# Kernel optimization log

Measured on AMD Instinct MI355X. Metric: run time of the kernel, lower is better.

The kernel has to match this reference:

```python
import jax, jax.numpy as jnp
import numpy as np

NHEAD = 12
EPS_Z = 1e-5
EPS_LN = 1e-5


def _zscore_last(t, n):
    # torch .std is unbiased (ddof=1)
    m = t.mean(axis=-1, keepdims=True)
    var = ((t - m) ** 2).sum(axis=-1, keepdims=True) / (n - 1)
    return (t - m) / (jnp.sqrt(var) + EPS_Z)


def _layernorm(x, g, b):
    m = x.mean(axis=-1, keepdims=True)
    v = ((x - m) ** 2).mean(axis=-1, keepdims=True)
    return (x - m) * jax.lax.rsqrt(v + EPS_LN) * g + b


def setup_inputs() -> dict:
    key = jax.random.key(0)
    ks = jax.random.split(key, 20)
    B, T, D, FF, E = 2, 1024, 768, 3072, 4
    p = lambda k, shape: (jax.random.normal(k, shape, jnp.float32) * 0.02)
    return {
        "src": jax.random.normal(ks[0], (B, T, D), jnp.float32),
        "frac": jax.random.uniform(ks[1], (B, T), jnp.float32),
        "Wq": p(ks[2], (D, D)), "bq": jnp.zeros((D,), jnp.float32),
        "Wk": p(ks[3], (D, D)), "bk": jnp.zeros((D,), jnp.float32),
        "Wv": p(ks[4], (D, D)), "bv": jnp.zeros((D,), jnp.float32),
        "Wo": p(ks[5], (D, D)), "bo": jnp.zeros((D,), jnp.float32),
        "gamma": jnp.float32(1.0),
        "ln1_g": jnp.ones((D,), jnp.float32), "ln1_b": jnp.zeros((D,), jnp.float32),
        "ln2_g": jnp.ones((D,), jnp.float32), "ln2_b": jnp.zeros((D,), jnp.float32),
        "Wg": p(ks[6], (E, D)), "bg": jnp.zeros((E,), jnp.float32),
        "W1": p(ks[7], (E, D, FF)), "b1": jnp.zeros((E, FF), jnp.float32),
        "W2": p(ks[8], (E, FF, D)), "b2": jnp.zeros((E, D), jnp.float32),
    }


def reference(src, frac, Wq, bq, Wk, bk, Wv, bv, Wo, bo, gamma,
              ln1_g, ln1_b, ln2_g, ln2_b, Wg, bg, W1, b1, W2, b2):
    B, T, D = src.shape
    H = NHEAD
    hd = D // H
    scale = hd ** -0.5

    # ---- attention (add_frac_bias=False path) ----
    Q = (src @ Wq.T + bq).reshape(B, T, H, hd)
    K = (src @ Wk.T + bk).reshape(B, T, H, hd)
    V = (src @ Wv.T + bv).reshape(B, T, H, hd)
    logits = jnp.einsum('bqhd,bkhd->bhqk', Q, K) * scale
    logits = gamma * _zscore_last(logits, T)
    probs = jax.nn.softmax(logits, axis=-1)
    attn = jnp.einsum('bhqk,bkhd->bqhd', probs, V).reshape(B, T, D)
    attn = attn @ Wo.T + bo

    # ---- residual + norm1 ----
    x = _layernorm(src + attn, ln1_g, ln1_b)

    # ---- MoE top-2 feed-forward ----
    E = Wg.shape[0]
    gate_scores = jax.nn.softmax(x @ Wg.T + bg, axis=-1)          # [B,T,E]
    top2_val, top2_idx = jax.lax.top_k(gate_scores, 2)            # [B,T,2]
    combine = (jax.nn.one_hot(top2_idx, E, dtype=x.dtype)
               * top2_val[..., None]).sum(axis=-2)                # [B,T,E]
    h = jax.nn.relu(jnp.einsum('btd,edf->ebtf', x, W1) + b1[:, None, None, :])
    y = jnp.einsum('ebtf,efd->ebtd', h, W2) + b2[:, None, None, :]
    ff = jnp.einsum('ebtd,bte->btd', y, combine)

    # ---- residual + norm2 ----
    return _layernorm(x + ff, ln2_g, ln2_b)
```

## Files before the change

kernel.cpp:

```cpp
#include <hip/hip_runtime.h>

typedef unsigned short u16;
typedef short bf16x8 __attribute__((ext_vector_type(8)));
typedef float f32x4 __attribute__((ext_vector_type(4)));

#define BB 2
#define TT 1024
#define DD 768
#define HH 12
#define HD 64
#define FFD 3072
#define NE 4
#define NTOK (BB*TT)
#define CROWS 4608
#define SLABZ 3538944L

#define MFMA16(a, b, c) __builtin_amdgcn_mfma_f32_16x16x32_bf16((a), (b), (c), 0, 0, 0)

#define ASYNC16(gsrc, ldst)                                                    \
    __builtin_amdgcn_global_load_lds(                                          \
        (const __attribute__((address_space(1))) void*)(gsrc),                 \
        (__attribute__((address_space(3))) void*)(ldst), 16, 0, 0)

__device__ __forceinline__ float us2f(u16 u) {
    return __uint_as_float(((unsigned int)u) << 16);
}
__device__ __forceinline__ u16 f2us(float f) {
    unsigned int x = __float_as_uint(f);
    x += 0x7fffu + ((x >> 16) & 1u);
    return (u16)(x >> 16);
}

__global__ __launch_bounds__(256) void convert5_kernel(
    const float* __restrict__ src, const float* __restrict__ wq,
    const float* __restrict__ wk, const float* __restrict__ wv,
    const float* __restrict__ wo,
    const float* __restrict__ bq, const float* __restrict__ bk,
    const float* __restrict__ bv,
    u16* __restrict__ src_h, u16* __restrict__ wqkv_h, u16* __restrict__ wo_h,
    float* __restrict__ bqkv)
{
    const int bid = blockIdx.x, tid = threadIdx.x;
    if (bid == 1920) {
        for (int i = tid; i < 3 * DD; i += 256) {
            float v = (i < DD) ? bq[i] : (i < 2 * DD) ? bk[i - DD] : bv[i - 2 * DD];
            bqkv[i] = v;
        }
        return;
    }
    int i = bid * 256 + tid;
    const float* in; u16* out; int off;
    if (i < 196608) { in = src; out = src_h; off = i; }
    else {
        int j = i - 196608; int w = j / 73728; off = j - w * 73728;
        in = (w == 0) ? wq : (w == 1) ? wk : (w == 2) ? wv : wo;
        out = (w < 3) ? wqkv_h + (size_t)w * (DD * DD) : wo_h;
    }
    const float4* p = reinterpret_cast<const float4*>(in) + (size_t)off * 2;
    float4 a = p[0], b = p[1];
    u16 o[8] = {f2us(a.x), f2us(a.y), f2us(a.z), f2us(a.w),
                f2us(b.x), f2us(b.y), f2us(b.z), f2us(b.w)};
    *reinterpret_cast<uint4*>(out + (size_t)off * 8) = *reinterpret_cast<uint4*>(o);
}

__global__ __launch_bounds__(256) void transpose_convert_kernel(
    const float* __restrict__ src, u16* __restrict__ dst,
    int C, int dstStride, long srcZ, long dstZ)
{
    __shared__ float tile[32][33];
    const float* s = src + (size_t)blockIdx.z * srcZ;
    u16* d = dst + (size_t)blockIdx.z * dstZ;
    const int c0 = blockIdx.x * 32, r0 = blockIdx.y * 32;
    const int tid = threadIdx.x;
    {
        const int r = tid >> 3, cs = (tid & 7) * 4;
        float4 v = *reinterpret_cast<const float4*>(&s[(size_t)(r0 + r) * C + c0 + cs]);
        tile[r][cs] = v.x; tile[r][cs + 1] = v.y;
        tile[r][cs + 2] = v.z; tile[r][cs + 3] = v.w;
    }
    __syncthreads();
    {
        const int c = tid >> 3, rs = (tid & 7) * 4;
        u16 o[4] = {f2us(tile[rs][c]), f2us(tile[rs + 1][c]),
                    f2us(tile[rs + 2][c]), f2us(tile[rs + 3][c])};
        *reinterpret_cast<uint2*>(&d[(size_t)(c0 + c) * dstStride + r0 + rs]) =
            *reinterpret_cast<uint2*>(o);
    }
}

__global__ __launch_bounds__(256) void scan_build_kernel(
    const int* __restrict__ epack, int* __restrict__ cnt,
    int* __restrict__ rowtok, int* __restrict__ tok2row)
{
    __shared__ int sc[256][4];
    const int tid = threadIdx.x;
    for (int i = tid; i < CROWS; i += 256) rowtok[i] = 0;
    int ep[8];
    int l0 = 0, l1 = 0, l2 = 0, l3 = 0;
    #pragma unroll
    for (int i = 0; i < 8; i++) {
        const int v = epack[tid * 8 + i];
        ep[i] = v;
        const int a = v & 15, b = (v >> 4) & 15;
        l0 += (a == 0) + (b == 0);
        l1 += (a == 1) + (b == 1);
        l2 += (a == 2) + (b == 2);
        l3 += (a == 3) + (b == 3);
    }
    sc[tid][0] = l0; sc[tid][1] = l1; sc[tid][2] = l2; sc[tid][3] = l3;
    __syncthreads();
    for (int off = 1; off < 256; off <<= 1) {
        int v0 = 0, v1 = 0, v2 = 0, v3 = 0;
        if (tid >= off) {
            v0 = sc[tid - off][0]; v1 = sc[tid - off][1];
            v2 = sc[tid - off][2]; v3 = sc[tid - off][3];
        }
        __syncthreads();
        if (tid >= off) {
            sc[tid][0] += v0; sc[tid][1] += v1;
            sc[tid][2] += v2; sc[tid][3] += v3;
        }
        __syncthreads();
    }
    const int t0 = sc[255][0], t1 = sc[255][1], t2 = sc[255][2], t3 = sc[255][3];
    if (tid == 0) { cnt[0] = t0; cnt[1] = t1; cnt[2] = t2; cnt[3] = t3; }
    const int b1 = (t0 + 127) & ~127;
    const int b2 = b1 + ((t1 + 127) & ~127);
    const int b3 = b2 + ((t2 + 127) & ~127);
    int r0 = sc[tid][0] - l0;
    int r1 = b1 + sc[tid][1] - l1;
    int r2 = b2 + sc[tid][2] - l2;
    int r3 = b3 + sc[tid][3] - l3;
    #pragma unroll
    for (int i = 0; i < 8; i++) {
        const int t = tid * 8 + i;
        const int a = ep[i] & 15, b = (ep[i] >> 4) & 15;
        const int ra = (a == 0) ? r0++ : (a == 1) ? r1++ : (a == 2) ? r2++ : r3++;
        rowtok[ra] = t; tok2row[t * 2] = ra;
        const int rb = (b == 0) ? r0++ : (b == 1) ? r1++ : (b == 2) ? r2++ : r3++;
        rowtok[rb] = t; tok2row[t * 2 + 1] = rb;
    }
}

__global__ __launch_bounds__(256) void gemm_bt_kernel(
    const u16* __restrict__ A, int lda, long aZ,
    const u16* __restrict__ Bt, int ldb, long bZ,
    int K, int mode, int swz,
    float* __restrict__ outF, u16* __restrict__ outH,
    u16* __restrict__ outH2, u16* __restrict__ outH3,
    int ldc, long cZ,
    const float* __restrict__ biasF, int biasZ,
    const int* __restrict__ rowtok, const int* __restrict__ cntp,
    const float* __restrict__ comb)
{
    __shared__ __align__(16) u16 As[128 * 64];
    __shared__ __align__(16) u16 Bs[128 * 64];
    const int tid = threadIdx.x;
    int bx, by, z, e = 0, baseE = 0;
    if (swz == 3) {
        const int fid = blockIdx.x;
        const int xcd = fid & 7; int r = fid >> 3;
        const int half = (r >= 96) ? 1 : 0; r -= half * 96;
        bx = r % 6; by = r / 6;
        const int ez = xcd * 2 + half; e = ez >> 2; z = ez & 3;
    } else if (swz == 1) {
        const int fid = blockIdx.x;
        const int xcd = fid & 7; const int r = fid >> 3;
        const int ne = xcd * 12 + (r % 12);
        by = r / 12; bx = ne % 24; e = ne / 24; z = e;
    } else {
        bx = blockIdx.x; by = blockIdx.y; z = blockIdx.z;
    }
    if (mode == 2 || mode == 4) {
        const int q0 = (cntp[0] + 127) & ~127;
        const int q1 = (cntp[1] + 127) & ~127;
        const int q2 = (cntp[2] + 127) & ~127;
        baseE = (e > 0 ? q0 : 0) + (e > 1 ? q1 : 0) + (e > 2 ? q2 : 0);
        if (by * 128 >= cntp[e]) return;
    }
    const int m0 = by * 128, n0 = bx * 128;
    const u16* Ab = A + (size_t)z * aZ;
    const u16* Bb = Bt + (size_t)z * bZ;
    if (mode == 4) {
        Ab += (size_t)baseE * lda;
        Bb += (size_t)e * ((size_t)DD * FFD);
    }

    const int wave = tid >> 6, lane = tid & 63;
    const int wm = (wave & 1) * 64, wn = (wave >> 1) * 64;
    const int fm = lane & 15;
    const int g  = lane >> 4;

    const int lr8 = lane >> 3;
    const int cg  = ((lane & 7) ^ lr8) * 8;
    const u16 *aG[4], *bG[4];
    u16 *aL[4], *bL[4];
    #pragma unroll
    for (int i = 0; i < 4; i++) {
        const int rr = wave * 32 + i * 8 + lr8;
        int arow;
        if (mode == 2) arow = rowtok[baseE + m0 + rr];
        else           arow = m0 + rr;
        aG[i] = Ab + (size_t)arow * lda + cg;
        bG[i] = Bb + (size_t)(n0 + rr) * ldb + cg;
        aL[i] = &As[(wave * 32 + i * 8) * 64];
        bL[i] = &Bs[(wave * 32 + i * 8) * 64];
    }

    const int c0 = ((g    ) ^ (fm & 7)) * 8;
    const int c1 = ((g + 4) ^ (fm & 7)) * 8;
    const u16* pa[4]; const u16* pb[4];
    #pragma unroll
    for (int i = 0; i < 4; i++) {
        pa[i] = &As[(wm + i * 16 + fm) * 64];
        pb[i] = &Bs[(wn + i * 16 + fm) * 64];
    }

    f32x4 acc[4][4] = {};

    for (int k0 = 0; k0 < K; k0 += 64) {
        #pragma unroll
        for (int i = 0; i < 4; i++) ASYNC16(aG[i] + k0, aL[i]);
        #pragma unroll
        for (int i = 0; i < 4; i++) ASYNC16(bG[i] + k0, bL[i]);
        __syncthreads();
        #pragma unroll
        for (int ks = 0; ks < 2; ks++) {
            const int cc = ks ? c1 : c0;
            bf16x8 af[4], bf[4];
            #pragma unroll
            for (int i = 0; i < 4; i++)
                af[i] = *reinterpret_cast<const bf16x8*>(pa[i] + cc);
            #pragma unroll
            for (int j = 0; j < 4; j++)
                bf[j] = *reinterpret_cast<const bf16x8*>(pb[j] + cc);
            #pragma unroll
            for (int i = 0; i < 4; i++)
                #pragma unroll
                for (int j = 0; j < 4; j++)
                    acc[i][j] = MFMA16(af[i], bf[j], acc[i][j]);
        }
        __syncthreads();
    }

    const int cn = lane & 15, cr = (lane >> 4) * 4;

    if (mode == 2) {
        u16* Cs = As;
        #pragma unroll
        for (int i = 0; i < 4; i++) {
            if (i) __syncthreads();
            int tokr[4]; float combr[4];
            #pragma unroll
            for (int r = 0; r < 4; r++)
                tokr[r] = rowtok[baseE + m0 + wm + i * 16 + cr + r];
            #pragma unroll
            for (int r = 0; r < 4; r++)
                combr[r] = comb[(size_t)tokr[r] * NE + z];
            #pragma unroll
            for (int j = 0; j < 4; j++) {
                const int n = n0 + wn + j * 16 + cn;
                const float bias = biasF[(size_t)z * biasZ + n];
                #pragma unroll
                for (int r = 0; r < 4; r++) {
                    float y = fmaxf(acc[i][j][r] + bias, 0.f) * combr[r];
                    Cs[((wave & 1) * 16 + cr + r) * 128 + wn + j * 16 + cn] = f2us(y);
                }
            }
            __syncthreads();
            const int lr2 = tid >> 3, c2 = (tid & 7) * 16;
            const int m2 = m0 + (lr2 >> 4) * 64 + i * 16 + (lr2 & 15);
            u16* dst = outH + (size_t)(baseE + m2) * ldc + n0 + c2;
            *reinterpret_cast<uint4*>(dst) =
                *reinterpret_cast<const uint4*>(&Cs[lr2 * 128 + c2]);
            *reinterpret_cast<uint4*>(dst + 8) =
                *reinterpret_cast<const uint4*>(&Cs[lr2 * 128 + c2 + 8]);
        }
        return;
    }

    #pragma unroll
    for (int i = 0; i < 4; i++) {
        #pragma unroll
        for (int j = 0; j < 4; j++) {
            const int n = n0 + wn + j * 16 + cn;
            #pragma unroll
            for (int r = 0; r < 4; r++) {
                const int m = m0 + wm + i * 16 + cr + r;
                float y = acc[i][j][r];
                if (mode == 0) {
                    y += biasF[n];
                    int which = (n >= 1536) ? 2 : (n >= 768 ? 1 : 0);
                    int nn = n - which * 768;
                    int bb = m >> 10, t = m & 1023;
                    int hh = nn >> 6, d = nn & 63;
                    if (which == 0)
                        outH[(((size_t)(bb * HH + hh) * TT + t) << 6) + d] = f2us(y);
                    else if (which == 1)
                        outH2[(((size_t)(bb * HH + hh) * TT + t) << 6) + d] = f2us(y);
                    else
                        outH3[(((size_t)(bb * HH + hh) * HD + d) << 10) + t] = f2us(y);
                } else {
                    float* basep = outF + (size_t)z * cZ;
                    basep[(size_t)(baseE + m) * ldc + n] = y;
                }
            }
        }
    }
}

#define PSTR 1032
__global__ __launch_bounds__(256, 2) void attn_mfma_kernel(
    const u16* __restrict__ Qh, const u16* __restrict__ Kh,
    const u16* __restrict__ VT, const float* __restrict__ gamma_p,
    u16* __restrict__ attn_out)
{
    __shared__ __align__(16) u16 P[32 * PSTR];
    __shared__ float wred[4][32][4];
    __shared__ float dred[4][32];
    __shared__ float aArr[32], cmArr[32], dinvArr[32];

    const int qt = blockIdx.x, bh = blockIdx.y;
    const int b = bh / HH, h = bh - b * HH;
    const int tid = threadIdx.x, wave = tid >> 6, lane = tid & 63;
    const int g = lane >> 4, fm = lane & 15;
    const float gamma = gamma_p[0];
    const int m0 = qt * 32;
    const u16* Qp = Qh + (size_t)bh * TT * HD;
    const u16* Kp = Kh + (size_t)bh * TT * HD;
    const u16* Vp = VT + (size_t)bh * HD * TT;

    bf16x8 af[2][2];
    #pragma unroll
    for (int mi = 0; mi < 2; mi++)
        #pragma unroll
        for (int ks = 0; ks < 2; ks++)
            af[mi][ks] = *reinterpret_cast<const bf16x8*>(
                Qp + (size_t)(m0 + mi * 16 + fm) * HD + ks * 32 + g * 8);

    const int n0w = wave * 256;
    f32x4 acc[16][2] = {};
    #pragma unroll
    for (int nj = 0; nj < 16; nj++) {
        const u16* kp = Kp + (size_t)(n0w + nj * 16 + fm) * HD + g * 8;
        bf16x8 b0 = *reinterpret_cast<const bf16x8*>(kp);
        bf16x8 b1 = *reinterpret_cast<const bf16x8*>(kp + 32);
        acc[nj][0] = MFMA16(af[0][0], b0, acc[nj][0]);
        acc[nj][0] = MFMA16(af[0][1], b1, acc[nj][0]);
        acc[nj][1] = MFMA16(af[1][0], b0, acc[nj][1]);
        acc[nj][1] = MFMA16(af[1][1], b1, acc[nj][1]);
    }

    #pragma unroll
    for (int mi = 0; mi < 2; mi++) {
        #pragma unroll
        for (int r = 0; r < 4; r++) {
            float s1 = 0.f, s2 = 0.f, mx = -3.4e38f, mn = 3.4e38f;
            #pragma unroll
            for (int nj = 0; nj < 16; nj++) {
                float v = acc[nj][mi][r];
                s1 += v; s2 = fmaf(v, v, s2);
                mx = fmaxf(mx, v); mn = fminf(mn, v);
            }
            #pragma unroll
            for (int msk = 1; msk < 16; msk <<= 1) {
                s1 += __shfl_xor(s1, msk);
                s2 += __shfl_xor(s2, msk);
                mx = fmaxf(mx, __shfl_xor(mx, msk));
                mn = fminf(mn, __shfl_xor(mn, msk));
            }
            if (fm == 0) {
                int row = mi * 16 + g * 4 + r;
                wred[wave][row][0] = s1; wred[wave][row][1] = s2;
                wred[wave][row][2] = mx; wred[wave][row][3] = mn;
            }
        }
    }
    __syncthreads();
    if (tid < 32) {
        float s1 = 0.f, s2 = 0.f, mx = -3.4e38f, mn = 3.4e38f;
        #pragma unroll
        for (int w = 0; w < 4; w++) {
            s1 += wred[w][tid][0]; s2 += wred[w][tid][1];
            mx = fmaxf(mx, wred[w][tid][2]); mn = fminf(mn, wred[w][tid][3]);
        }
        float var = (s2 - s1 * s1 * (1.f / TT)) * (1.f / (TT - 1));
        var = fmaxf(var, 0.f);
        float a = gamma / (sqrtf(var) + 8e-5f);
        aArr[tid] = a;
        cmArr[tid] = (a >= 0.f) ? a * mx : a * mn;
    }
    __syncthreads();

    #pragma unroll
    for (int mi = 0; mi < 2; mi++) {
        #pragma unroll
        for (int r = 0; r < 4; r++) {
            const int row = mi * 16 + g * 4 + r;
            const float a = aArr[row], cm = cmArr[row];
            float dp = 0.f;
            #pragma unroll
            for (int nj = 0; nj < 16; nj++) {
                float p = __expf(fmaf(a, acc[nj][mi][r], -cm));
                u16 pb = f2us(p);
                dp += us2f(pb);
                P[row * PSTR + n0w + nj * 16 + fm] = pb;
            }
            #pragma unroll
            for (int msk = 1; msk < 16; msk <<= 1) dp += __shfl_xor(dp, msk);
            if (fm == 0) dred[wave][row] = dp;
        }
    }
    __syncthreads();
    if (tid < 32)
        dinvArr[tid] = 1.f / (dred[0][tid] + dred[1][tid] + dred[2][tid] + dred[3][tid]);
    __syncthreads();

    f32x4 oacc[2] = {};
    #pragma unroll 4
    for (int ks = 0; ks < 32; ks++) {
        bf16x8 bv = *reinterpret_cast<const bf16x8*>(
            Vp + (size_t)(wave * 16 + fm) * TT + ks * 32 + g * 8);
        bf16x8 a0 = *reinterpret_cast<const bf16x8*>(&P[(size_t)fm * PSTR + ks * 32 + g * 8]);
        bf16x8 a1 = *reinterpret_cast<const bf16x8*>(&P[(size_t)(16 + fm) * PSTR + ks * 32 + g * 8]);
        oacc[0] = MFMA16(a0, bv, oacc[0]);
        oacc[1] = MFMA16(a1, bv, oacc[1]);
    }
    #pragma unroll
    for (int mi = 0; mi < 2; mi++) {
        #pragma unroll
        for (int r = 0; r < 4; r++) {
            int row = mi * 16 + g * 4 + r;
            int t = m0 + row;
            attn_out[((size_t)(b * TT + t)) * DD + h * HD + wave * 16 + fm] =
                f2us(oacc[mi][r] * dinvArr[row]);
        }
    }
}

__global__ __launch_bounds__(256) void ln1_kernel(
    const float* __restrict__ p0, const float* __restrict__ p1,
    const float* __restrict__ p2, const float* __restrict__ p3,
    const float* __restrict__ src, const float* __restrict__ bo,
    const float* __restrict__ g, const float* __restrict__ bta,
    const float* __restrict__ Wg, const float* __restrict__ bg,
    float* __restrict__ outF, u16* __restrict__ outH,
    float* __restrict__ comb, int* __restrict__ epack)
{
    const int row = blockIdx.x, tid = threadIdx.x;
    __shared__ float red[256];
    __shared__ float gred[4][4];
    const size_t base = (size_t)row * DD;
    float v[3];
    #pragma unroll
    for (int i = 0; i < 3; i++) {
        int c = tid + i * 256;
        v[i] = p0[base + c] + p1[base + c] + p2[base + c] + p3[base + c]
             + src[base + c] + bo[c];
    }
    float s = v[0] + v[1] + v[2];
    red[tid] = s; __syncthreads();
    #pragma unroll
    for (int o = 128; o > 0; o >>= 1) { if (tid < o) red[tid] += red[tid + o]; __syncthreads(); }
    const float mean = red[0] * (1.f / 768.f);
    __syncthreads();
    float qv = 0.f;
    #pragma unroll
    for (int i = 0; i < 3; i++) { float d = v[i] - mean; qv += d * d; }
    red[tid] = qv; __syncthreads();
    #pragma unroll
    for (int o = 128; o > 0; o >>= 1) { if (tid < o) red[tid] += red[tid + o]; __syncthreads(); }
    const float var = red[0] * (1.f / 768.f);
    const float rs = rsqrtf(var + 1e-5f);
    float ga0 = 0.f, ga1 = 0.f, ga2 = 0.f, ga3 = 0.f;
    #pragma unroll
    for (int i = 0; i < 3; i++) {
        int c = tid + i * 256;
        float o = (v[i] - mean) * rs * g[c] + bta[c];
        outF[base + c] = o;
        outH[base + c] = f2us(o);
        ga0 = fmaf(o, Wg[c], ga0);
        ga1 = fmaf(o, Wg[DD + c], ga1);
        ga2 = fmaf(o, Wg[2 * DD + c], ga2);
        ga3 = fmaf(o, Wg[3 * DD + c], ga3);
    }
    #pragma unroll
    for (int off = 32; off > 0; off >>= 1) {
        ga0 += __shfl_down(ga0, off, 64);
        ga1 += __shfl_down(ga1, off, 64);
        ga2 += __shfl_down(ga2, off, 64);
        ga3 += __shfl_down(ga3, off, 64);
    }
    const int wave = tid >> 6, lane = tid & 63;
    if (lane == 0) {
        gred[wave][0] = ga0; gred[wave][1] = ga1;
        gred[wave][2] = ga2; gred[wave][3] = ga3;
    }
    __syncthreads();
    if (tid == 0) {
        float gg[NE];
        #pragma unroll
        for (int e = 0; e < NE; e++)
            gg[e] = gred[0][e] + gred[1][e] + gred[2][e] + gred[3][e] + bg[e];
        float m = -1e30f;
        #pragma unroll
        for (int e = 0; e < NE; e++) m = fmaxf(m, gg[e]);
        float ex[NE], ssum = 0.f;
        #pragma unroll
        for (int e = 0; e < NE; e++) { ex[e] = __expf(gg[e] - m); ssum += ex[e]; }
        #pragma unroll
        for (int e = 0; e < NE; e++) ex[e] /= ssum;
        int e1 = 0;
        #pragma unroll
        for (int e = 1; e < NE; e++) if (ex[e] > ex[e1]) e1 = e;
        int e2 = -1;
        #pragma unroll
        for (int e = 0; e < NE; e++) if (e != e1 && (e2 < 0 || ex[e] > ex[e2])) e2 = e;
        float c[NE] = {0.f, 0.f, 0.f, 0.f};
        c[e1] = ex[e1]; c[e2] = ex[e2];
        #pragma unroll
        for (int e = 0; e < NE; e++) comb[(size_t)row * NE + e] = c[e];
        epack[row] = e1 | (e2 << 4);
    }
}

__global__ __launch_bounds__(256) void ln2_kernel(
    const float* __restrict__ x, const float* __restrict__ pslab,
    const int* __restrict__ tok2row,
    const float* __restrict__ comb, const float* __restrict__ b2,
    const float* __restrict__ g, const float* __restrict__ bta,
    float* __restrict__ outF)
{
    const int row = blockIdx.x, tid = threadIdx.x;
    __shared__ float red[256];
    const size_t base = (size_t)row * DD;
    const int r0 = tok2row[row * 2], r1 = tok2row[row * 2 + 1];
    const float* q0 = pslab + (size_t)r0 * DD;
    const float* q1 = pslab + (size_t)r1 * DD;
    const float c0 = comb[row * NE + 0], c1 = comb[row * NE + 1];
    const float c2 = comb[row * NE + 2], c3 = comb[row * NE + 3];
    float v[3];
    #pragma unroll
    for (int i = 0; i < 3; i++) {
        int c = tid + i * 256;
        float t = x[base + c];
        t += q0[c] + q0[SLABZ + c] + q0[2 * SLABZ + c] + q0[3 * SLABZ + c];
        t += q1[c] + q1[SLABZ + c] + q1[2 * SLABZ + c] + q1[3 * SLABZ + c];
        t = fmaf(c0, b2[c], t);
        t = fmaf(c1, b2[DD + c], t);
        t = fmaf(c2, b2[2 * DD + c], t);
        t = fmaf(c3, b2[3 * DD + c], t);
        v[i] = t;
    }
    float s = v[0] + v[1] + v[2];
    red[tid] = s; __syncthreads();
    #pragma unroll
    for (int o = 128; o > 0; o >>= 1) { if (tid < o) red[tid] += red[tid + o]; __syncthreads(); }
    const float mean = red[0] * (1.f / 768.f);
    __syncthreads();
    float qv = 0.f;
    #pragma unroll
    for (int i = 0; i < 3; i++) { float d = v[i] - mean; qv += d * d; }
    red[tid] = qv; __syncthreads();
    #pragma unroll
    for (int o = 128; o > 0; o >>= 1) { if (tid < o) red[tid] += red[tid + o]; __syncthreads(); }
    const float var = red[0] * (1.f / 768.f);
    const float rs = rsqrtf(var + 1e-5f);
    #pragma unroll
    for (int i = 0; i < 3; i++) {
        int c = tid + i * 256;
        outF[base + c] = (v[i] - mean) * rs * g[c] + bta[c];
    }
}

extern "C" void kernel_launch(void* const* d_in, const int* in_sizes, int n_in,
                              void* d_out, int out_size, void* d_ws, size_t ws_size,
                              hipStream_t stream)
{
    const float* src  = (const float*)d_in[0];
    const float* Wq   = (const float*)d_in[2];  const float* bq = (const float*)d_in[3];
    const float* Wk   = (const float*)d_in[4];  const float* bk = (const float*)d_in[5];
    const float* Wv   = (const float*)d_in[6];  const float* bv = (const float*)d_in[7];
    const float* Wo   = (const float*)d_in[8];  const float* bo = (const float*)d_in[9];
    const float* gam  = (const float*)d_in[10];
    const float* ln1g = (const float*)d_in[11]; const float* ln1b = (const float*)d_in[12];
    const float* ln2g = (const float*)d_in[13]; const float* ln2b = (const float*)d_in[14];
    const float* Wg   = (const float*)d_in[15]; const float* bg = (const float*)d_in[16];
    const float* W1   = (const float*)d_in[17]; const float* b1 = (const float*)d_in[18];
    const float* W2   = (const float*)d_in[19]; const float* b2 = (const float*)d_in[20];
    (void)ws_size; (void)in_sizes; (void)n_in; (void)out_size;

    char* ws = (char*)d_ws;
    u16*   W1T  = (u16*)(ws);
    float* wop  = (float*)(ws + 18874368);
    float* pslab= (float*)(ws);
    u16*   W2T  = (u16*)(ws + 56623104);
    u16*   hb   = (u16*)(ws + 75497472);
    float* x    = (float*)(ws + 103809024);
    u16*   xh   = (u16*)(ws + 110100480);
    float* comb = (float*)(ws + 113246208);
    float* bqkv = (float*)(ws + 113278976);
    int*   cnt    = (int*)(ws + 113288192);
    int*   rowtok = (int*)(ws + 113288256);
    int*   epack  = (int*)(ws + 113306688);
    int*   tok2row= (int*)(ws + 113323072);
    char* H = ws + 75497472;
    u16*   Qh     = (u16*)(H);
    u16*   Kh     = (u16*)(H + 3145728);
    u16*   VTh    = (u16*)(H + 6291456);
    u16*   src_h  = (u16*)(H + 9437184);
    u16*   attn_h = (u16*)(H + 12582912);
    u16*   WqkvH  = (u16*)(H + 15728640);
    u16*   WoH    = (u16*)(H + 19267584);
    const long PZ = (long)NTOK * DD;

    convert5_kernel<<<1921, 256, 0, stream>>>(
        src, Wq, Wk, Wv, Wo, bq, bk, bv, src_h, WqkvH, WoH, bqkv);
    transpose_convert_kernel<<<dim3(FFD / 32, DD / 32, NE), 256, 0, stream>>>(
        W1, W1T, FFD, DD, (long)DD * FFD, (long)FFD * DD);
    transpose_convert_kernel<<<dim3(DD / 32, FFD / 32, NE), 256, 0, stream>>>(
        W2, W2T, DD, FFD, (long)FFD * DD, (long)FFD * DD);

    gemm_bt_kernel<<<dim3(2304 / 128, NTOK / 128, 1), 256, 0, stream>>>(
        src_h, DD, 0, WqkvH, DD, 0, DD, 0, 0,
        nullptr, Qh, Kh, VTh, 0, 0, bqkv, 0, nullptr, nullptr, nullptr);

    attn_mfma_kernel<<<dim3(TT / 32, BB * HH), 256, 0, stream>>>(
        Qh, Kh, VTh, gam, attn_h);

    gemm_bt_kernel<<<dim3(DD / 128, NTOK / 128, 4), 256, 0, stream>>>(
        attn_h, DD, 192L, WoH, DD, 192L, 192, 3, 0,
        wop, nullptr, nullptr, nullptr, DD, PZ, nullptr, 0, nullptr, nullptr, nullptr);

    ln1_kernel<<<NTOK, 256, 0, stream>>>(
        wop, wop + PZ, wop + 2 * PZ, wop + 3 * PZ, src, bo,
        ln1g, ln1b, Wg, bg, x, xh, comb, epack);

    scan_build_kernel<<<1, 256, 0, stream>>>(epack, cnt, rowtok, tok2row);

    gemm_bt_kernel<<<dim3(1536, 1, 1), 256, 0, stream>>>(
        xh, DD, 0, W1T, DD, (long)FFD * DD, DD, 2, 1,
        nullptr, hb, nullptr, nullptr, FFD, 0, b1, FFD, rowtok, cnt, comb);

    gemm_bt_kernel<<<dim3(1536, 1, 1), 256, 0, stream>>>(
        hb, FFD, 768L, W2T, FFD, 768L, 768, 4, 3,
        pslab, nullptr, nullptr, nullptr, DD, SLABZ, nullptr, 0, rowtok, cnt, nullptr);

    ln2_kernel<<<NTOK, 256, 0, stream>>>(
        x, pslab, tok2row, comb, b2, ln2g, ln2b, (float*)d_out);
}
```

Before: 369.5 us.

## Double-buffer LDS in QKV/out-proj GEMMs, coalesce QKV epilogue, XCD-aware tile mapping

Result: faster. 343.6 us (-7.0%).

```diff
diff --git a/kernel.cpp b/kernel.cpp
--- a/kernel.cpp
+++ b/kernel.cpp
@@ -142,6 +142,7 @@
     }
 }
 
+template<int DB>
 __global__ __launch_bounds__(256) void gemm_bt_kernel(
     const u16* __restrict__ A, int lda, long aZ,
     const u16* __restrict__ Bt, int ldb, long bZ,
@@ -153,8 +154,8 @@
     const int* __restrict__ rowtok, const int* __restrict__ cntp,
     const float* __restrict__ comb)
 {
-    __shared__ __align__(16) u16 As[128 * 64];
-    __shared__ __align__(16) u16 Bs[128 * 64];
+    __shared__ __align__(16) u16 As[(DB ? 2 : 1) * 128 * 64];
+    __shared__ __align__(16) u16 Bs[(DB ? 2 : 1) * 128 * 64];
     const int tid = threadIdx.x;
     int bx, by, z, e = 0, baseE = 0;
     if (swz == 3) {
@@ -168,6 +169,10 @@
         const int xcd = fid & 7; const int r = fid >> 3;
         const int ne = xcd * 12 + (r % 12);
         by = r / 12; bx = ne % 24; e = ne / 24; z = e;
+    } else if (swz == 2) {
+        const int fid = blockIdx.x;
+        const int g = (fid & 7) * 36 + (fid >> 3);
+        by = g & 15; bx = g >> 4; z = 0;
     } else {
         bx = blockIdx.x; by = blockIdx.y; z = blockIdx.z;
     }
@@ -207,6 +212,14 @@
         bL[i] = &Bs[(wave * 32 + i * 8) * 64];
     }
 
+#define STAGE(B, KO) do {                                                      \
+        const int _o = (B) * (128 * 64);                                       \
+        _Pragma("unroll")                                                      \
+        for (int _i = 0; _i < 4; _i++) ASYNC16(aG[_i] + (KO), aL[_i] + _o);    \
+        _Pragma("unroll")                                                      \
+        for (int _i = 0; _i < 4; _i++) ASYNC16(bG[_i] + (KO), bL[_i] + _o);    \
+    } while (0)
+
     const int c0 = ((g    ) ^ (fm & 7)) * 8;
     const int c1 = ((g + 4) ^ (fm & 7)) * 8;
     const u16* pa[4]; const u16* pb[4];
@@ -217,16 +230,23 @@
     }
 
     f32x4 acc[4][4] = {};
+    int buf = 0;
+    if (DB) STAGE(0, 0);
 
     for (int k0 = 0; k0 < K; k0 += 64) {
-        #pragma unroll
-        for (int i = 0; i < 4; i++) ASYNC16(aG[i] + k0, aL[i]);
-        #pragma unroll
-        for (int i = 0; i < 4; i++) ASYNC16(bG[i] + k0, bL[i]);
-        __syncthreads();
+        if (DB) {
+            asm volatile("s_waitcnt vmcnt(0)" ::: "memory");
+            __builtin_amdgcn_s_barrier();
+            __builtin_amdgcn_sched_barrier(0);
+            if (k0 + 64 < K) STAGE(buf ^ 1, k0 + 64);
+        } else {
+            STAGE(0, k0);
+            __syncthreads();
+        }
+        const int bo = DB ? buf * (128 * 64) : 0;
         #pragma unroll
         for (int ks = 0; ks < 2; ks++) {
-            const int cc = ks ? c1 : c0;
+            const int cc = bo + (ks ? c1 : c0);
             bf16x8 af[4], bf[4];
             #pragma unroll
             for (int i = 0; i < 4; i++)
@@ -240,10 +260,61 @@
                 for (int j = 0; j < 4; j++)
                     acc[i][j] = MFMA16(af[i], bf[j], acc[i][j]);
         }
-        __syncthreads();
-    }
+        if (DB) buf ^= 1;
+        else    __syncthreads();
+    }
+    if (DB) __syncthreads();
+#undef STAGE
 
     const int cn = lane & 15, cr = (lane >> 4) * 4;
+
+    if (mode == 0) {
+        const int which = (n0 >= 1536) ? 2 : (n0 >= 768 ? 1 : 0);
+        const int nb = n0 - which * 768;
+        u16* outP = (which == 0) ? outH : (which == 1) ? outH2 : outH3;
+        u16* Cs = As;
+        #pragma unroll
+        for (int i = 0; i < 4; i++) {
+            if (i) __syncthreads();
+            #pragma unroll
+            for (int j = 0; j < 4; j++) {
+                const int n = n0 + wn + j * 16 + cn;
+                const float bias = biasF[n];
+                #pragma unroll
+                for (int r = 0; r < 4; r++) {
+                    Cs[((wave & 1) * 16 + cr + r) * 128 + wn + j * 16 + cn] =
+                        f2us(acc[i][j][r] + bias);
+                }
+            }
+            __syncthreads();
+            if (which < 2) {
+                const int lr2 = tid >> 3, c2 = (tid & 7) * 16;
+                const int m2 = m0 + (lr2 >> 4) * 64 + i * 16 + (lr2 & 15);
+                const int bb2 = m2 >> 10, t2 = m2 & 1023;
+                const int hh = (nb + c2) >> 6, d0 = (nb + c2) & 63;
+                u16* dst = outP + (((size_t)(bb2 * HH + hh) * TT + t2) << 6) + d0;
+                *reinterpret_cast<uint4*>(dst) =
+                    *reinterpret_cast<const uint4*>(&Cs[lr2 * 128 + c2]);
+                *reinterpret_cast<uint4*>(dst + 8) =
+                    *reinterpret_cast<const uint4*>(&Cs[lr2 * 128 + c2 + 8]);
+            } else {
+                const int nl = tid >> 1, half = tid & 1;
+                const int hh = (nb + nl) >> 6, d = (nb + nl) & 63;
+                #pragma unroll
+                for (int seg = 0; seg < 2; seg++) {
+                    u16 o[8];
+                    #pragma unroll
+                    for (int k = 0; k < 8; k++)
+                        o[k] = Cs[(seg * 16 + half * 8 + k) * 128 + nl];
+                    const int t0 = m0 + seg * 64 + i * 16 + half * 8;
+                    const int bb2 = t0 >> 10, tt2 = t0 & 1023;
+                    u16* dst = outP + (((size_t)(bb2 * HH + hh) * HD + d) << 10) + tt2;
+                    *reinterpret_cast<uint4*>(dst) = *reinterpret_cast<uint4*>(o);
+                }
+            }
+        }
+        return;
+    }
 
     if (mode == 2) {
         u16* Cs = As;
@@ -287,23 +358,8 @@
             #pragma unroll
             for (int r = 0; r < 4; r++) {
                 const int m = m0 + wm + i * 16 + cr + r;
-                float y = acc[i][j][r];
-                if (mode == 0) {
-                    y += biasF[n];
-                    int which = (n >= 1536) ? 2 : (n >= 768 ? 1 : 0);
-                    int nn = n - which * 768;
-                    int bb = m >> 10, t = m & 1023;
-                    int hh = nn >> 6, d = nn & 63;
-                    if (which == 0)
-                        outH[(((size_t)(bb * HH + hh) * TT + t) << 6) + d] = f2us(y);
-                    else if (which == 1)
-                        outH2[(((size_t)(bb * HH + hh) * TT + t) << 6) + d] = f2us(y);
-                    else
-                        outH3[(((size_t)(bb * HH + hh) * HD + d) << 10) + t] = f2us(y);
-                } else {
-                    float* basep = outF + (size_t)z * cZ;
-                    basep[(size_t)(baseE + m) * ldc + n] = y;
-                }
+                float* basep = outF + (size_t)z * cZ;
+                basep[(size_t)(baseE + m) * ldc + n] = acc[i][j][r];
             }
         }
     }
@@ -621,14 +677,14 @@
     transpose_convert_kernel<<<dim3(DD / 32, FFD / 32, NE), 256, 0, stream>>>(
         W2, W2T, DD, FFD, (long)FFD * DD, (long)FFD * DD);
 
-    gemm_bt_kernel<<<dim3(2304 / 128, NTOK / 128, 1), 256, 0, stream>>>(
-        src_h, DD, 0, WqkvH, DD, 0, DD, 0, 0,
+    gemm_bt_kernel<1><<<dim3(288, 1, 1), 256, 0, stream>>>(
+        src_h, DD, 0, WqkvH, DD, 0, DD, 0, 2,
         nullptr, Qh, Kh, VTh, 0, 0, bqkv, 0, nullptr, nullptr, nullptr);
 
     attn_mfma_kernel<<<dim3(TT / 32, BB * HH), 256, 0, stream>>>(
         Qh, Kh, VTh, gam, attn_h);
 
-    gemm_bt_kernel<<<dim3(DD / 128, NTOK / 128, 4), 256, 0, stream>>>(
+    gemm_bt_kernel<1><<<dim3(DD / 128, NTOK / 128, 4), 256, 0, stream>>>(
         attn_h, DD, 192L, WoH, DD, 192L, 192, 3, 0,
         wop, nullptr, nullptr, nullptr, DD, PZ, nullptr, 0, nullptr, nullptr, nullptr);
 
@@ -638,11 +694,11 @@
 
     scan_build_kernel<<<1, 256, 0, stream>>>(epack, cnt, rowtok, tok2row);
 
-    gemm_bt_kernel<<<dim3(1536, 1, 1), 256, 0, stream>>>(
+    gemm_bt_kernel<0><<<dim3(1536, 1, 1), 256, 0, stream>>>(
         xh, DD, 0, W1T, DD, (long)FFD * DD, DD, 2, 1,
         nullptr, hb, nullptr, nullptr, FFD, 0, b1, FFD, rowtok, cnt, comb);
 
-    gemm_bt_kernel<<<dim3(1536, 1, 1), 256, 0, stream>>>(
+    gemm_bt_kernel<0><<<dim3(1536, 1, 1), 256, 0, stream>>>(
         hb, FFD, 768L, W2T, FFD, 768L, 768, 4, 3,
         pslab, nullptr, nullptr, nullptr, DD, SLABZ, nullptr, 0, rowtok, cnt, nullptr);
 
```
